# Kernel tuning notes

Measured on AMD Instinct MI355X. Metric: run time of the kernel, lower is better.

The kernel has to match this reference:

```python
import jax, jax.numpy as jnp
import numpy as np

N_HEAD = 16


def setup_inputs() -> dict:
    key = jax.random.key(0)
    ks = jax.random.split(key, 6)
    B, T, H = 4, 2048, 1024
    inp = jax.random.normal(ks[0], (B, T, H), dtype=jnp.float32)
    # padding mask: valid prefix of random length in [T//2, T] per batch row
    lengths = jax.random.randint(ks[1], (B, 1), T // 2, T + 1)
    mask = jnp.arange(T)[None, :] < lengths  # (B, T) bool
    s = 0.02
    w_qkv = jax.random.normal(ks[2], (H, 3 * H), dtype=jnp.float32) * s
    b_qkv = jax.random.normal(ks[3], (3 * H,), dtype=jnp.float32) * s
    w_out = jax.random.normal(ks[4], (H, H), dtype=jnp.float32) * s
    b_out = jax.random.normal(ks[5], (H,), dtype=jnp.float32) * s
    return {"input": inp, "mask": mask, "w_qkv": w_qkv, "b_qkv": b_qkv,
            "w_out": w_out, "b_out": b_out}


def reference(input, mask, w_qkv, b_qkv, w_out, b_out):
    B, T, H = input.shape
    hd = H // N_HEAD
    qkv = input @ w_qkv + b_qkv                       # (B, T, 3H)
    q, k, v = jnp.split(qkv, 3, axis=-1)
    # (B, T, H) -> (B, nh, T, hd)
    q = q.reshape(B, T, N_HEAD, hd).transpose(0, 2, 1, 3)
    k = k.reshape(B, T, N_HEAD, hd).transpose(0, 2, 1, 3)
    v = v.reshape(B, T, N_HEAD, hd).transpose(0, 2, 1, 3)
    scores = jnp.einsum('bhqd,bhkd->bhqk', q, k) / jnp.sqrt(jnp.float32(hd))
    causal = jnp.tril(jnp.ones((T, T), dtype=bool))   # (T, T)
    full_mask = causal[None, None, :, :] & mask[:, None, None, :]  # (B,1,T,T) bcast over heads
    scores = jnp.where(full_mask, scores, -jnp.inf)
    attn = jax.nn.softmax(scores, axis=-1)            # (B, nh, T, T)
    o = jnp.einsum('bhqk,bhkd->bhqd', attn, v)        # (B, nh, T, hd)
    o = o.transpose(0, 2, 1, 3).reshape(B, T, H)
    return o @ w_out + b_out
```

## Files before the change

kernel.cpp:

```cpp
#include <hip/hip_runtime.h>
#include <math.h>

#define B_  4
#define T_  2048
#define H_  1024
#define NH  16
#define HD  64
#define H3  3072

typedef short bf16x8 __attribute__((ext_vector_type(8)));
typedef short bf16x4 __attribute__((ext_vector_type(4)));
typedef float f32x4  __attribute__((ext_vector_type(4)));
typedef float f32x16 __attribute__((ext_vector_type(16)));

#define SC2F 0.18033688011112042f

__device__ __forceinline__ unsigned short f2bf(float f) {
    union { float f; unsigned u; } v; v.f = f;
    unsigned u = v.u;
    unsigned r = (u + 0x7fffu + ((u >> 16) & 1u)) >> 16;
    return (unsigned short)r;
}

__device__ __forceinline__ void gload_lds16(const void* g, void* l) {
    __builtin_amdgcn_global_load_lds(
        (const __attribute__((address_space(1))) unsigned*)g,
        (__attribute__((address_space(3))) unsigned*)l, 16, 0, 0);
}

__device__ __forceinline__ f32x4 mfma_16x16x16_bf16(bf16x4 a, bf16x4 b, f32x4 c) {
#if __has_builtin(__builtin_amdgcn_mfma_f32_16x16x16_bf16)
    return __builtin_amdgcn_mfma_f32_16x16x16_bf16(a, b, c, 0, 0, 0);
#elif __has_builtin(__builtin_amdgcn_mfma_f32_16x16x16bf16_1k)
    return __builtin_amdgcn_mfma_f32_16x16x16bf16_1k(a, b, c, 0, 0, 0);
#else
    f32x4 d;
    asm volatile("v_mfma_f32_16x16x16_bf16 %0, %1, %2, %3"
                 : "=v"(d) : "v"(a), "v"(b), "v"(c));
    return d;
#endif
}

__global__ __launch_bounds__(256) void prep_kernel(
    const float* __restrict__ X, unsigned short* __restrict__ Xbf,
    const float* __restrict__ Wqkv, unsigned short* __restrict__ WqkvT,
    const float* __restrict__ Wout, unsigned short* __restrict__ WoutT)
{
    int bid = blockIdx.x;
    int t = threadIdx.x;
    if (bid < 4096) {
        __shared__ unsigned short tile[32][33];
        int bxx = bid & 127, byy = bid >> 7;
        const float* in;
        unsigned short* out;
        int N, nb;
        if (bxx < 96) { in = Wqkv; out = WqkvT; N = H3; nb = bxx * 32; }
        else          { in = Wout; out = WoutT; N = H_; nb = (bxx - 96) * 32; }
        int kb = byy * 32;
        int tx = t & 31, ty = t >> 5;
        for (int i = 0; i < 32; i += 8)
            tile[ty + i][tx] = f2bf(in[(long)(kb + ty + i) * N + nb + tx]);
        __syncthreads();
        for (int i = 0; i < 32; i += 8)
            out[(long)(nb + ty + i) * H_ + kb + tx] = tile[tx][ty + i];
    } else {
        long u = (long)(bid - 4096) * 256 + t;
#pragma unroll
        for (int j = 0; j < 4; j++) {
            long i = (u + (long)j * 524288) * 4;
            float4 v = *(const float4*)(X + i);
            ushort4 o;
            o.x = f2bf(v.x); o.y = f2bf(v.y); o.z = f2bf(v.z); o.w = f2bf(v.w);
            *(ushort4*)(Xbf + i) = o;
        }
    }
}

__global__ __launch_bounds__(256) void gemm_qkv_kernel(
    const unsigned short* __restrict__ A,
    const unsigned short* __restrict__ Bt,
    const float* __restrict__ bias,
    unsigned short* __restrict__ C,
    unsigned short* __restrict__ Vt)
{
    const int K = H_, N = H3;
    __shared__ unsigned short Asm[128][64];
    __shared__ unsigned short Bsm[128][64];

    int tn = blockIdx.x * 128, tm = blockIdx.y * 128;
    int tid = threadIdx.x;
    int wid = tid >> 6, lane = tid & 63;
    int l31 = lane & 31, lh = lane >> 5;
    int wm = (wid & 1) * 64, wn = (wid >> 1) * 64;

    int rl = lane >> 3;
    int g8 = ((lane & 7) ^ rl) * 8;
    const unsigned short* aP = A  + (long)(tm + wid * 32 + rl) * K + g8;
    const unsigned short* bP = Bt + (long)(tn + wid * 32 + rl) * K + g8;
    int rk = l31 & 7;

    f32x16 acc[2][2] = {};

    for (int k0 = 0; k0 < K; k0 += 64) {
        __syncthreads();
#pragma unroll
        for (int t = 0; t < 4; t++)
            gload_lds16(aP + (long)(t * 8) * K + k0, &Asm[wid * 32 + t * 8][0]);
#pragma unroll
        for (int t = 0; t < 4; t++)
            gload_lds16(bP + (long)(t * 8) * K + k0, &Bsm[wid * 32 + t * 8][0]);
        __syncthreads();

#pragma unroll
        for (int ks = 0; ks < 4; ks++) {
            int pc = ((ks * 2 + lh) ^ rk) * 8;
            bf16x8 af[2], bv[2];
            af[0] = *(const bf16x8*)(&Asm[wm + l31][pc]);
            af[1] = *(const bf16x8*)(&Asm[wm + 32 + l31][pc]);
            bv[0] = *(const bf16x8*)(&Bsm[wn + l31][pc]);
            bv[1] = *(const bf16x8*)(&Bsm[wn + 32 + l31][pc]);
#pragma unroll
            for (int i = 0; i < 2; i++)
#pragma unroll
                for (int j = 0; j < 2; j++)
                    acc[i][j] = __builtin_amdgcn_mfma_f32_32x32x16_bf16(
                        af[i], bv[j], acc[i][j], 0, 0, 0);
        }
    }

    if (tn >= 2 * H_) {
#pragma unroll
        for (int i = 0; i < 2; i++)
#pragma unroll
            for (int j = 0; j < 2; j++) {
                int col = tn + wn + j * 32 + l31;
                float bs = bias[col];
                int feat = col - 2 * H_;
#pragma unroll
                for (int rg = 0; rg < 4; rg++) {
                    int tok0 = tm + wm + i * 32 + rg * 8 + lh * 4;
                    int bb = tok0 >> 11;
                    unsigned d0 = (unsigned)f2bf(acc[i][j][rg * 4 + 0] + bs) |
                                  ((unsigned)f2bf(acc[i][j][rg * 4 + 1] + bs) << 16);
                    unsigned d1 = (unsigned)f2bf(acc[i][j][rg * 4 + 2] + bs) |
                                  ((unsigned)f2bf(acc[i][j][rg * 4 + 3] + bs) << 16);
                    unsigned short* dst = Vt + ((long)(bb * 1024 + feat)) * T_ + (tok0 & (T_ - 1));
                    *(uint2*)dst = make_uint2(d0, d1);
                }
            }
        return;
    }

#pragma unroll
    for (int i = 0; i < 2; i++)
#pragma unroll
        for (int j = 0; j < 2; j++) {
            int col = tn + wn + j * 32 + l31;
            float bs = bias[col];
            bool ks_ = (col >= H_) && (col < 2 * H_);
#pragma unroll
            for (int r = 0; r < 16; r++) {
                int row = tm + wm + i * 32 + (r & 3) + 8 * (r >> 2) + 4 * lh;
                float v = acc[i][j][r] + bs;
                if (ks_) v *= SC2F;
                C[(long)row * N + col] = f2bf(v);
            }
        }
}

template <int TN>
__global__ __launch_bounds__(256) void gemm_kernel(
    const unsigned short* __restrict__ A,
    const unsigned short* __restrict__ Bt,
    const float* __restrict__ bias,
    float* __restrict__ C,
    int M, int N, int K)
{
    __shared__ unsigned short Asm[2][128][64];
    __shared__ unsigned short Bsm[2][TN][64];

    int nbx = gridDim.x;
    int bid = blockIdx.y * nbx + blockIdx.x;
    int cpx = (nbx * gridDim.y) >> 3;
    int lin = (bid & 7) * cpx + (bid >> 3);
    int bx = lin % nbx, by = lin / nbx;

    int tn = bx * TN, tm = by * 128;
    int tid = threadIdx.x;
    int wid = tid >> 6, lane = tid & 63;
    int l31 = lane & 31, lh = lane >> 5;
    int wm = (wid & 1) * 64, wn = (wid >> 1) * (TN / 2);

    int rl = lane >> 3;
    int g8 = ((lane & 7) ^ rl) * 8;
    const unsigned short* aP = A  + (long)(tm + wid * 32 + rl) * K + g8;
    const unsigned short* bP = Bt + (long)(tn + wid * (TN / 4) + rl) * K + g8;
    int rk = l31 & 7;

    f32x16 acc[2][TN / 64] = {};

#pragma unroll
    for (int t = 0; t < 4; t++)
        gload_lds16(aP + (long)(t * 8) * K, &Asm[0][wid * 32 + t * 8][0]);
#pragma unroll
    for (int t = 0; t < TN / 32; t++)
        gload_lds16(bP + (long)(t * 8) * K, &Bsm[0][wid * (TN / 4) + t * 8][0]);

    int cur = 0;
    for (int k0 = 0; k0 < K; k0 += 64) {
        __syncthreads();
        if (k0 + 64 < K) {
#pragma unroll
            for (int t = 0; t < 4; t++)
                gload_lds16(aP + (long)(t * 8) * K + k0 + 64, &Asm[cur ^ 1][wid * 32 + t * 8][0]);
#pragma unroll
            for (int t = 0; t < TN / 32; t++)
                gload_lds16(bP + (long)(t * 8) * K + k0 + 64, &Bsm[cur ^ 1][wid * (TN / 4) + t * 8][0]);
        }
#pragma unroll
        for (int ks = 0; ks < 4; ks++) {
            int pc = ((ks * 2 + lh) ^ rk) * 8;
            bf16x8 af[2], bv[TN / 64];
            af[0] = *(const bf16x8*)(&Asm[cur][wm + l31][pc]);
            af[1] = *(const bf16x8*)(&Asm[cur][wm + 32 + l31][pc]);
#pragma unroll
            for (int j = 0; j < TN / 64; j++)
                bv[j] = *(const bf16x8*)(&Bsm[cur][wn + j * 32 + l31][pc]);
#pragma unroll
            for (int i = 0; i < 2; i++)
#pragma unroll
                for (int j = 0; j < TN / 64; j++)
                    acc[i][j] = __builtin_amdgcn_mfma_f32_32x32x16_bf16(
                        af[i], bv[j], acc[i][j], 0, 0, 0);
        }
        cur ^= 1;
    }

#pragma unroll
    for (int i = 0; i < 2; i++)
#pragma unroll
        for (int j = 0; j < TN / 64; j++) {
            int col = tn + wn + j * 32 + l31;
            float bs = bias[col];
#pragma unroll
            for (int r = 0; r < 16; r++) {
                int row = tm + wm + i * 32 + (r & 3) + 8 * (r >> 2) + 4 * lh;
                C[(long)row * N + col] = acc[i][j][r] + bs;
            }
        }
}

__global__ __launch_bounds__(256) void attn_kernel(
    const unsigned short* __restrict__ QKV,
    const unsigned short* __restrict__ Vt,
    const void* __restrict__ mask,
    unsigned short* __restrict__ O)
{
    int idx = blockIdx.x;
    int bh = idx & 63;
    int qt = 15 - (idx >> 6);
    int b = bh >> 4, h = bh & 15;
    int q0 = qt * 128;

    int tid = threadIdx.x;
    int wid = tid >> 6, lane = tid & 63, quad = lane >> 4, lr = lane & 15;
    int quad4 = quad * 4;

    int len;
    {
        const unsigned* mu = (const unsigned*)mask;
        bool is_byte = (mu[0] == 0x01010101u);
        int cnt = 0;
        if (is_byte) {
            const unsigned char* m8 = (const unsigned char*)mask;
            for (int i = lane; i < T_; i += 64) cnt += (m8[b * T_ + i] != 0);
        } else {
            const unsigned* m32 = (const unsigned*)mask;
            for (int i = lane; i < T_; i += 64) cnt += (m32[b * T_ + i] != 0);
        }
        cnt += __shfl_xor(cnt, 1);  cnt += __shfl_xor(cnt, 2);
        cnt += __shfl_xor(cnt, 4);  cnt += __shfl_xor(cnt, 8);
        cnt += __shfl_xor(cnt, 16); cnt += __shfl_xor(cnt, 32);
        len = cnt;
    }

    __shared__ __align__(16) unsigned short SH[16384];
    unsigned short (*Kd)[64][64] = (unsigned short (*)[64][64])(&SH[0]);
    unsigned short (*Vd)[64][64] = (unsigned short (*)[64][64])(&SH[8192]);

    const long qkv_base = (long)b * T_ * H3;

    bf16x8 qf[2][2];
#pragma unroll
    for (int nq = 0; nq < 2; nq++)
#pragma unroll
        for (int ks = 0; ks < 2; ks++)
            qf[nq][ks] = *(const bf16x8*)(QKV + qkv_base +
                (long)(q0 + wid * 32 + nq * 16 + lr) * H3 + h * HD + ks * 32 + quad * 8);

    int rl = lane >> 3;
    int g8 = ((lane & 7) ^ rl) * 8;
    const unsigned short* kB = QKV + qkv_base + (long)(wid * 16 + rl) * H3 + H_ + h * HD + g8;
    const unsigned short* vB = Vt + (long)(bh * 64 + wid * 16 + rl) * T_ + g8;

    f32x4 lacc[2] = {};
    f32x4 Oacc[4][2] = {};

    int kmax = min(q0 + 127, len - 1);
    int n_kt = (kmax >> 6) + 1;
    int q_wave_lo = q0 + wid * 32;
    int qwl_u = __builtin_amdgcn_readfirstlane(q_wave_lo);
    int q_wave_hi = qwl_u + 31;
    int bnd_[2] = { min(q_wave_lo + lr, len - 1),
                    min(q_wave_lo + 16 + lr, len - 1) };
    int rk = lr & 7;

    const short oneb = (short)0x3F80;
    bf16x4 vones = { oneb, oneb, oneb, oneb };

#pragma unroll
    for (int t = 0; t < 2; t++) {
        gload_lds16(kB + (long)(t * 8) * H3, &Kd[0][wid * 16 + t * 8][0]);
        gload_lds16(vB + (long)(t * 8) * T_, &Vd[0][wid * 16 + t * 8][0]);
    }

    for (int kt = 0; kt < n_kt; kt++) {
        int cur = kt & 1;
        __syncthreads();

        if (kt + 1 < n_kt) {
            long koff = (long)((kt + 1) * 64) * H3;
            int voff = (kt + 1) * 64;
#pragma unroll
            for (int t = 0; t < 2; t++) {
                gload_lds16(kB + koff + (long)(t * 8) * H3, &Kd[cur ^ 1][wid * 16 + t * 8][0]);
                gload_lds16(vB + (long)(t * 8) * T_ + voff, &Vd[cur ^ 1][wid * 16 + t * 8][0]);
            }
        }

        int k_lo = kt * 64;
        if (k_lo > q_wave_hi || k_lo >= len) continue;

        int mt_hi = min(q_wave_hi, len - 1);
        int nmt = min(4, ((mt_hi - k_lo) >> 4) + 1);
        nmt = __builtin_amdgcn_readfirstlane(nmt);

        f32x4 Sacc[4][2] = {};
        __builtin_amdgcn_s_setprio(1);
#pragma unroll
        for (int mt = 0; mt < 4; mt++) {
            if (mt >= nmt) continue;
#pragma unroll
            for (int ks = 0; ks < 2; ks++) {
                bf16x8 kf = *(const bf16x8*)(&Kd[cur][mt * 16 + lr][((ks * 4 + quad) ^ rk) * 8]);
                Sacc[mt][0] = __builtin_amdgcn_mfma_f32_16x16x32_bf16(kf, qf[0][ks], Sacc[mt][0], 0, 0, 0);
                Sacc[mt][1] = __builtin_amdgcn_mfma_f32_16x16x32_bf16(kf, qf[1][ks], Sacc[mt][1], 0, 0, 0);
            }
        }
        __builtin_amdgcn_s_setprio(0);

        unsigned pkk[4][2][2];
#pragma unroll
        for (int mt = 0; mt < 4; mt++) {
            if (mt >= nmt) continue;
            int kb0 = k_lo + mt * 16;
            int kbl = kb0 + quad4;
#pragma unroll
            for (int nq = 0; nq < 2; nq++) {
                float p[4];
                if (kb0 + 15 <= qwl_u + nq * 16 && kb0 + 15 < len) {
#pragma unroll
                    for (int r = 0; r < 4; r++)
                        p[r] = __builtin_amdgcn_exp2f(Sacc[mt][nq][r]);
                } else {
                    int dlt = bnd_[nq] - kbl;
#pragma unroll
                    for (int r = 0; r < 4; r++) {
                        float s = (r <= dlt) ? Sacc[mt][nq][r] : -INFINITY;
                        p[r] = __builtin_amdgcn_exp2f(s);
                    }
                }
                pkk[mt][nq][0] = __builtin_amdgcn_perm(__float_as_uint(p[1]), __float_as_uint(p[0]), 0x07060302);
                pkk[mt][nq][1] = __builtin_amdgcn_perm(__float_as_uint(p[3]), __float_as_uint(p[2]), 0x07060302);
            }
        }

        __builtin_amdgcn_s_setprio(1);
#pragma unroll
        for (int mt = 0; mt < 4; mt++) {
            if (mt >= nmt) continue;
            union { unsigned u[2]; bf16x4 v; } bu[2];
            bu[0].u[0] = pkk[mt][0][0]; bu[0].u[1] = pkk[mt][0][1];
            bu[1].u[0] = pkk[mt][1][0]; bu[1].u[1] = pkk[mt][1][1];
            lacc[0] = mfma_16x16x16_bf16(vones, bu[0].v, lacc[0]);
            lacc[1] = mfma_16x16x16_bf16(vones, bu[1].v, lacc[1]);
#pragma unroll
            for (int md = 0; md < 4; md++) {
                bf16x4 vf = *(const bf16x4*)(&Vd[cur][md * 16 + lr]
                    [((mt * 2 + (quad >> 1)) ^ rk) * 8 + (quad & 1) * 4]);
                Oacc[md][0] = mfma_16x16x16_bf16(vf, bu[0].v, Oacc[md][0]);
                Oacc[md][1] = mfma_16x16x16_bf16(vf, bu[1].v, Oacc[md][1]);
            }
        }
        __builtin_amdgcn_s_setprio(0);
    }

    __syncthreads();
    {
        unsigned short (*Es)[68] = (unsigned short (*)[68])(&SH[0]);
        float inv[2] = { 1.f / lacc[0][0], 1.f / lacc[1][0] };
#pragma unroll
        for (int nq = 0; nq < 2; nq++)
#pragma unroll
            for (int md = 0; md < 4; md++)
#pragma unroll
                for (int rp = 0; rp < 2; rp++) {
                    float e0 = Oacc[md][nq][rp * 2]     * inv[nq];
                    float e1 = Oacc[md][nq][rp * 2 + 1] * inv[nq];
                    unsigned w = __builtin_amdgcn_perm(__float_as_uint(e1), __float_as_uint(e0), 0x07060302);
                    *(unsigned*)(&Es[wid * 32 + nq * 16 + lr][md * 16 + quad * 4 + rp * 2]) = w;
                }
        __asm__ volatile("s_waitcnt lgkmcnt(0)" ::: "memory");
        int row = lane >> 1, cb = (lane & 1) * 32;
        long tok = (long)b * T_ + q0 + wid * 32 + row;
#pragma unroll
        for (int i = 0; i < 4; i++) {
            float4 v = *(const float4*)(&Es[wid * 32 + row][cb + i * 8]);
            *(float4*)(&O[tok * H_ + h * HD + cb + i * 8]) = v;
        }
    }
}

extern "C" void kernel_launch(void* const* d_in, const int* in_sizes, int n_in,
                              void* d_out, int out_size, void* d_ws, size_t ws_size,
                              hipStream_t stream) {
    const float* X    = (const float*)d_in[0];
    const void*  mask = d_in[1];
    const float* Wqkv = (const float*)d_in[2];
    const float* bqkv = (const float*)d_in[3];
    const float* Wout = (const float*)d_in[4];
    const float* bout = (const float*)d_in[5];

    char* ws = (char*)d_ws;
    unsigned short* WqkvT = (unsigned short*)(ws + 256);
    unsigned short* WoutT = WqkvT + (long)H3 * H_;
    unsigned short* QKV   = WoutT + (long)H_ * H_;
    unsigned short* Xbf   = QKV + (long)B_ * T_ * H3;
    unsigned short* Vt    = Xbf + (long)B_ * T_ * H_;
    unsigned short* Obf   = Xbf;

    const int M = B_ * T_;

    prep_kernel<<<6144, 256, 0, stream>>>(X, Xbf, Wqkv, WqkvT, Wout, WoutT);
    gemm_qkv_kernel<<<dim3(H3 / 128, M / 128), 256, 0, stream>>>(
        Xbf, WqkvT, bqkv, QKV, Vt);
    attn_kernel<<<B_ * NH * (T_ / 128), 256, 0, stream>>>(QKV, Vt, mask, Obf);
    gemm_kernel<64><<<dim3(H_ / 64, M / 128), 256, 0, stream>>>(
        Obf, WoutT, bout, (float*)d_out, M, H_, H_);
}
```

Measured before the change: 266.2 us.

## Pair causal query tiles per block to balance work and share K/V loads

Each attention block now handles two query tiles, the late tile (15-pr) and its mirror early tile (pr), so every block does the same amount of causal work. The grid is halved to 512 blocks. Each K/V tile staged in LDS is reused by both query tiles up to the early tile's range. The cost is roughly double the accumulator registers (two Oacc/lacc sets plus two sets of Q fragments), which may lower occupancy. Fewer blocks also means less parallelism across the CUs.

```diff
diff --git a/kernel.cpp b/kernel.cpp
--- a/kernel.cpp
+++ b/kernel.cpp
@@ -258,9 +258,9 @@
 {
     int idx = blockIdx.x;
     int bh = idx & 63;
-    int qt = 15 - (idx >> 6);
+    int pr = idx >> 6;
     int b = bh >> 4, h = bh & 15;
-    int q0 = qt * 128;
+    int q0_[2] = { (15 - pr) * 128, pr * 128 };
 
     int tid = threadIdx.x;
     int wid = tid >> 6, lane = tid & 63, quad = lane >> 4, lr = lane & 15;
@@ -290,29 +290,36 @@
 
     const long qkv_base = (long)b * T_ * H3;
 
-    bf16x8 qf[2][2];
-#pragma unroll
-    for (int nq = 0; nq < 2; nq++)
-#pragma unroll
-        for (int ks = 0; ks < 2; ks++)
-            qf[nq][ks] = *(const bf16x8*)(QKV + qkv_base +
-                (long)(q0 + wid * 32 + nq * 16 + lr) * H3 + h * HD + ks * 32 + quad * 8);
+    bf16x8 qf[2][2][2];
+#pragma unroll
+    for (int tt = 0; tt < 2; tt++)
+#pragma unroll
+        for (int nq = 0; nq < 2; nq++)
+#pragma unroll
+            for (int ks = 0; ks < 2; ks++)
+                qf[tt][nq][ks] = *(const bf16x8*)(QKV + qkv_base +
+                    (long)(q0_[tt] + wid * 32 + nq * 16 + lr) * H3 + h * HD + ks * 32 + quad * 8);
 
     int rl = lane >> 3;
     int g8 = ((lane & 7) ^ rl) * 8;
     const unsigned short* kB = QKV + qkv_base + (long)(wid * 16 + rl) * H3 + H_ + h * HD + g8;
     const unsigned short* vB = Vt + (long)(bh * 64 + wid * 16 + rl) * T_ + g8;
 
-    f32x4 lacc[2] = {};
-    f32x4 Oacc[4][2] = {};
-
-    int kmax = min(q0 + 127, len - 1);
-    int n_kt = (kmax >> 6) + 1;
-    int q_wave_lo = q0 + wid * 32;
-    int qwl_u = __builtin_amdgcn_readfirstlane(q_wave_lo);
-    int q_wave_hi = qwl_u + 31;
-    int bnd_[2] = { min(q_wave_lo + lr, len - 1),
-                    min(q_wave_lo + 16 + lr, len - 1) };
+    f32x4 lacc[2][2] = {};
+    f32x4 Oacc[2][4][2] = {};
+
+    int qwl[2], qwh[2], nkt[2], bndv[2][2];
+#pragma unroll
+    for (int tt = 0; tt < 2; tt++) {
+        int q_wave_lo = q0_[tt] + wid * 32;
+        qwl[tt] = __builtin_amdgcn_readfirstlane(q_wave_lo);
+        qwh[tt] = qwl[tt] + 31;
+        bndv[tt][0] = min(q_wave_lo + lr, len - 1);
+        bndv[tt][1] = min(q_wave_lo + 16 + lr, len - 1);
+        int kmax = min(q0_[tt] + 127, len - 1);
+        nkt[tt] = (kmax >> 6) + 1;
+    }
+    int n_kt = nkt[0];
     int rk = lr & 7;
 
     const short oneb = (short)0x3F80;
@@ -339,94 +346,105 @@
         }
 
         int k_lo = kt * 64;
-        if (k_lo > q_wave_hi || k_lo >= len) continue;
-
-        int mt_hi = min(q_wave_hi, len - 1);
-        int nmt = min(4, ((mt_hi - k_lo) >> 4) + 1);
-        nmt = __builtin_amdgcn_readfirstlane(nmt);
-
-        f32x4 Sacc[4][2] = {};
-        __builtin_amdgcn_s_setprio(1);
-#pragma unroll
-        for (int mt = 0; mt < 4; mt++) {
-            if (mt >= nmt) continue;
-#pragma unroll
-            for (int ks = 0; ks < 2; ks++) {
-                bf16x8 kf = *(const bf16x8*)(&Kd[cur][mt * 16 + lr][((ks * 4 + quad) ^ rk) * 8]);
-                Sacc[mt][0] = __builtin_amdgcn_mfma_f32_16x16x32_bf16(kf, qf[0][ks], Sacc[mt][0], 0, 0, 0);
-                Sacc[mt][1] = __builtin_amdgcn_mfma_f32_16x16x32_bf16(kf, qf[1][ks], Sacc[mt][1], 0, 0, 0);
-            }
-        }
-        __builtin_amdgcn_s_setprio(0);
-
-        unsigned pkk[4][2][2];
-#pragma unroll
-        for (int mt = 0; mt < 4; mt++) {
-            if (mt >= nmt) continue;
-            int kb0 = k_lo + mt * 16;
-            int kbl = kb0 + quad4;
-#pragma unroll
-            for (int nq = 0; nq < 2; nq++) {
-                float p[4];
-                if (kb0 + 15 <= qwl_u + nq * 16 && kb0 + 15 < len) {
-#pragma unroll
-                    for (int r = 0; r < 4; r++)
-                        p[r] = __builtin_amdgcn_exp2f(Sacc[mt][nq][r]);
-                } else {
-                    int dlt = bnd_[nq] - kbl;
-#pragma unroll
-                    for (int r = 0; r < 4; r++) {
-                        float s = (r <= dlt) ? Sacc[mt][nq][r] : -INFINITY;
-                        p[r] = __builtin_amdgcn_exp2f(s);
+
+#pragma unroll
+        for (int tt = 0; tt < 2; tt++) {
+            if (kt >= nkt[tt]) continue;
+            if (k_lo > qwh[tt] || k_lo >= len) continue;
+
+            int mt_hi = min(qwh[tt], len - 1);
+            int nmt = min(4, ((mt_hi - k_lo) >> 4) + 1);
+            nmt = __builtin_amdgcn_readfirstlane(nmt);
+
+            f32x4 Sacc[4][2] = {};
+            __builtin_amdgcn_s_setprio(1);
+#pragma unroll
+            for (int mt = 0; mt < 4; mt++) {
+                if (mt >= nmt) continue;
+#pragma unroll
+                for (int ks = 0; ks < 2; ks++) {
+                    bf16x8 kf = *(const bf16x8*)(&Kd[cur][mt * 16 + lr][((ks * 4 + quad) ^ rk) * 8]);
+                    Sacc[mt][0] = __builtin_amdgcn_mfma_f32_16x16x32_bf16(kf, qf[tt][0][ks], Sacc[mt][0], 0, 0, 0);
+                    Sacc[mt][1] = __builtin_amdgcn_mfma_f32_16x16x32_bf16(kf, qf[tt][1][ks], Sacc[mt][1], 0, 0, 0);
+                }
+            }
+            __builtin_amdgcn_s_setprio(0);
+
+            unsigned pkk[4][2][2];
+#pragma unroll
+            for (int mt = 0; mt < 4; mt++) {
+                if (mt >= nmt) continue;
+                int kb0 = k_lo + mt * 16;
+                int kbl = kb0 + quad4;
+#pragma unroll
+                for (int nq = 0; nq < 2; nq++) {
+                    float p[4];
+                    if (kb0 + 15 <= qwl[tt] + nq * 16 && kb0 + 15 < len) {
+#pragma unroll
+                        for (int r = 0; r < 4; r++)
+                            p[r] = __builtin_amdgcn_exp2f(Sacc[mt][nq][r]);
+                    } else {
+                        int dlt = bndv[tt][nq] - kbl;
+#pragma unroll
+                        for (int r = 0; r < 4; r++) {
+                            float s = (r <= dlt) ? Sacc[mt][nq][r] : -INFINITY;
+                            p[r] = __builtin_amdgcn_exp2f(s);
+                        }
                     }
+                    pkk[mt][nq][0] = __builtin_amdgcn_perm(__float_as_uint(p[1]), __float_as_uint(p[0]), 0x07060302);
+                    pkk[mt][nq][1] = __builtin_amdgcn_perm(__float_as_uint(p[3]), __float_as_uint(p[2]), 0x07060302);
                 }
-                pkk[mt][nq][0] = __builtin_amdgcn_perm(__float_as_uint(p[1]), __float_as_uint(p[0]), 0x07060302);
-                pkk[mt][nq][1] = __builtin_amdgcn_perm(__float_as_uint(p[3]), __float_as_uint(p[2]), 0x07060302);
-            }
-        }
-
-        __builtin_amdgcn_s_setprio(1);
-#pragma unroll
-        for (int mt = 0; mt < 4; mt++) {
-            if (mt >= nmt) continue;
-            union { unsigned u[2]; bf16x4 v; } bu[2];
-            bu[0].u[0] = pkk[mt][0][0]; bu[0].u[1] = pkk[mt][0][1];
-            bu[1].u[0] = pkk[mt][1][0]; bu[1].u[1] = pkk[mt][1][1];
-            lacc[0] = mfma_16x16x16_bf16(vones, bu[0].v, lacc[0]);
-            lacc[1] = mfma_16x16x16_bf16(vones, bu[1].v, lacc[1]);
-#pragma unroll
-            for (int md = 0; md < 4; md++) {
-                bf16x4 vf = *(const bf16x4*)(&Vd[cur][md * 16 + lr]
-                    [((mt * 2 + (quad >> 1)) ^ rk) * 8 + (quad & 1) * 4]);
-                Oacc[md][0] = mfma_16x16x16_bf16(vf, bu[0].v, Oacc[md][0]);
-                Oacc[md][1] = mfma_16x16x16_bf16(vf, bu[1].v, Oacc[md][1]);
-            }
-        }
-        __builtin_amdgcn_s_setprio(0);
+            }
+
+            __builtin_amdgcn_s_setprio(1);
+#pragma unroll
+            for (int mt = 0; mt < 4; mt++) {
+                if (mt >= nmt) continue;
+                union { unsigned u[2]; bf16x4 v; } bu[2];
+                bu[0].u[0] = pkk[mt][0][0]; bu[0].u[1] = pkk[mt][0][1];
+                bu[1].u[0] = pkk[mt][1][0]; bu[1].u[1] = pkk[mt][1][1];
+                lacc[tt][0] = mfma_16x16x16_bf16(vones, bu[0].v, lacc[tt][0]);
+                lacc[tt][1] = mfma_16x16x16_bf16(vones, bu[1].v, lacc[tt][1]);
+#pragma unroll
+                for (int md = 0; md < 4; md++) {
+                    bf16x4 vf = *(const bf16x4*)(&Vd[cur][md * 16 + lr]
+                        [((mt * 2 + (quad >> 1)) ^ rk) * 8 + (quad & 1) * 4]);
+                    Oacc[tt][md][0] = mfma_16x16x16_bf16(vf, bu[0].v, Oacc[tt][md][0]);
+                    Oacc[tt][md][1] = mfma_16x16x16_bf16(vf, bu[1].v, Oacc[tt][md][1]);
+                }
+            }
+            __builtin_amdgcn_s_setprio(0);
+        }
     }
 
     __syncthreads();
     {
         unsigned short (*Es)[68] = (unsigned short (*)[68])(&SH[0]);
-        float inv[2] = { 1.f / lacc[0][0], 1.f / lacc[1][0] };
-#pragma unroll
-        for (int nq = 0; nq < 2; nq++)
-#pragma unroll
-            for (int md = 0; md < 4; md++)
-#pragma unroll
-                for (int rp = 0; rp < 2; rp++) {
-                    float e0 = Oacc[md][nq][rp * 2]     * inv[nq];
-                    float e1 = Oacc[md][nq][rp * 2 + 1] * inv[nq];
-                    unsigned w = __builtin_amdgcn_perm(__float_as_uint(e1), __float_as_uint(e0), 0x07060302);
-                    *(unsigned*)(&Es[wid * 32 + nq * 16 + lr][md * 16 + quad * 4 + rp * 2]) = w;
-                }
-        __asm__ volatile("s_waitcnt lgkmcnt(0)" ::: "memory");
-        int row = lane >> 1, cb = (lane & 1) * 32;
-        long tok = (long)b * T_ + q0 + wid * 32 + row;
-#pragma unroll
-        for (int i = 0; i < 4; i++) {
-            float4 v = *(const float4*)(&Es[wid * 32 + row][cb + i * 8]);
-            *(float4*)(&O[tok * H_ + h * HD + cb + i * 8]) = v;
+#pragma unroll
+        for (int tt = 0; tt < 2; tt++) {
+            float inv[2] = { 1.f / lacc[tt][0][0], 1.f / lacc[tt][1][0] };
+#pragma unroll
+            for (int nq = 0; nq < 2; nq++)
+#pragma unroll
+                for (int md = 0; md < 4; md++)
+#pragma unroll
+                    for (int rp = 0; rp < 2; rp++) {
+                        float e0 = Oacc[tt][md][nq][rp * 2]     * inv[nq];
+                        float e1 = Oacc[tt][md][nq][rp * 2 + 1] * inv[nq];
+                        unsigned w = __builtin_amdgcn_perm(__float_as_uint(e1), __float_as_uint(e0), 0x07060302);
+                        *(unsigned*)(&Es[wid * 32 + nq * 16 + lr][md * 16 + quad * 4 + rp * 2]) = w;
+                    }
+            __asm__ volatile("s_waitcnt lgkmcnt(0)" ::: "memory");
+            __builtin_amdgcn_sched_barrier(0);
+            int row = lane >> 1, cb = (lane & 1) * 32;
+            long tok = (long)b * T_ + q0_[tt] + wid * 32 + row;
+#pragma unroll
+            for (int i = 0; i < 4; i++) {
+                float4 v = *(const float4*)(&Es[wid * 32 + row][cb + i * 8]);
+                *(float4*)(&O[tok * H_ + h * HD + cb + i * 8]) = v;
+            }
+            __asm__ volatile("s_waitcnt lgkmcnt(0)" ::: "memory");
+            __builtin_amdgcn_sched_barrier(0);
         }
     }
 }
@@ -454,7 +472,7 @@
     prep_kernel<<<6144, 256, 0, stream>>>(X, Xbf, Wqkv, WqkvT, Wout, WoutT);
     gemm_qkv_kernel<<<dim3(H3 / 128, M / 128), 256, 0, stream>>>(
         Xbf, WqkvT, bqkv, QKV, Vt);
-    attn_kernel<<<B_ * NH * (T_ / 128), 256, 0, stream>>>(QKV, Vt, mask, Obf);
+    attn_kernel<<<B_ * NH * 8, 256, 0, stream>>>(QKV, Vt, mask, Obf);
     gemm_kernel<64><<<dim3(H_ / 64, M / 128), 256, 0, stream>>>(
         Obf, WoutT, bout, (float*)d_out, M, H_, H_);
 }
```

Result: slower. 277.7 us (+4.3%).
